# Performance work log

Measured on AMD Instinct MI355X. Metric: run time of the kernel, lower is better.

Reference implementation:

```python
import jax, jax.numpy as jnp
import numpy as np

B, IN, OUT, D = 8192, 1024, 1024, 8


def setup_inputs() -> dict:
    key = jax.random.key(0)
    k1, k2, k3, k4 = jax.random.split(key, 4)
    # kaiming-uniform-ish init for weights, uniform for biases (values don't affect correctness)
    bound = 1.0 / np.sqrt(IN)
    return {
        "input": jax.random.normal(k1, (B, IN), dtype=jnp.float32),
        "w": jax.random.uniform(k2, (B, D), dtype=jnp.float32),
        "weights": jax.random.uniform(k3, (D, OUT, IN), dtype=jnp.float32, minval=-bound, maxval=bound),
        "biases": jax.random.uniform(k4, (D, OUT), dtype=jnp.float32, minval=-bound, maxval=bound),
    }


def reference(input, w, weights, biases):
    # Original math: weight[b] = sum_d w[b,d] * weights[d]  (shape [out,in])
    #                out[b]    = input[b] @ weight[b].T + sum_d w[b,d]*biases[d]
    # Restructured as one big GEMM + cheap dsize reduction:
    # tmp[b,d,o] = sum_i input[b,i] * weights[d,o,i]   (GEMM: [B,in] x [in, d*out])
    tmp = jnp.einsum('bi,doi->bdo', input, weights)
    out = jnp.einsum('bdo,bd->bo', tmp, w) + w @ biases
    return out
```

## Files before the change

kernel.cpp:

```cpp
#include <hip/hip_runtime.h>
#include <stdint.h>

typedef unsigned short u16;
typedef float v4f __attribute__((ext_vector_type(4)));
typedef short v8s __attribute__((ext_vector_type(8)));

#define B_   8192
#define IN_  1024
#define OUT_ 1024
#define D_   8

#define BM 128
#define BN 128
#define BK 64
#define KROW (D_ * IN_)

__device__ __forceinline__ u16 f2bf(float f) {
  uint32_t u = __float_as_uint(f);
  u += 0x7fffu + ((u >> 16) & 1u);
  return (u16)(u >> 16);
}

__global__ __launch_bounds__(256) void prep_fused(
    const float* __restrict__ input, const float* __restrict__ w,
    const float* __restrict__ weights,
    u16* __restrict__ aS, u16* __restrict__ wtBf) {
  const int bid = blockIdx.x;
  const int tid = threadIdx.x;
  if (bid < 8192) {
    const int b  = bid;
    const int i4 = tid;
    float4 v = ((const float4*)(input + (size_t)b * IN_))[i4];
    const float* wr_ = w + (size_t)b * D_;
    ushort4* dst = (ushort4*)aS + (size_t)b * (KROW / 4);
#pragma unroll
    for (int d = 0; d < D_; ++d) {
      const float s = wr_[d];
      ushort4 o;
      o.x = f2bf(s * v.x); o.y = f2bf(s * v.y);
      o.z = f2bf(s * v.z); o.w = f2bf(s * v.w);
      dst[d * (IN_ / 4) + i4] = o;
    }
  } else {
    int idx = (bid - 8192) * 256 + tid;
    float4 v = ((const float4*)weights)[idx];
    ushort4 o;
    o.x = f2bf(v.x); o.y = f2bf(v.y); o.z = f2bf(v.z); o.w = f2bf(v.w);
    ((ushort4*)wtBf)[idx] = o;
  }
}

__device__ __forceinline__ void gload_lds16(const u16* g, u16* l) {
  typedef __attribute__((address_space(1))) void gvoid;
  typedef __attribute__((address_space(3))) void lvoid;
  __builtin_amdgcn_global_load_lds((gvoid*)g, (lvoid*)l, 16, 0, 0);
}

__global__ __launch_bounds__(256) void gemm_main(
    const u16* __restrict__ A,
    const u16* __restrict__ Wt,
    const float* __restrict__ w,
    const float* __restrict__ biases,
    float* __restrict__ out) {
  __shared__ __align__(16) u16 As[BM * BK];
  __shared__ __align__(16) u16 Bs[BN * BK];

  const int id   = blockIdx.x;
  const int xcd  = id & 7;
  const int slot = id >> 3;
  const int by   = xcd + ((slot & 7) << 3);
  const int bx   = slot >> 3;

  const int tid  = threadIdx.x;
  const int wid  = tid >> 6;
  const int lane = tid & 63;
  const int wr   = wid >> 1, wc = wid & 1;
  const int quad = lane >> 4, l16 = lane & 15;
  const int m0   = by * BM;
  const int n0   = bx * BN;

  const int swz  = (lane & 7) ^ ((lane >> 3) & 7);
  const int rowS = wid * 32 + (lane >> 3);
  const u16* aBase[4];
  const u16* bBase[4];
  u16* lA[4];
  u16* lB[4];
#pragma unroll
  for (int j = 0; j < 4; ++j) {
    const int row = rowS + j * 8;
    aBase[j] = A  + (size_t)(m0 + row) * KROW + swz * 8;
    bBase[j] = Wt + (size_t)(n0 + row) * IN_  + swz * 8;
    const int c = wid * 256 + j * 64 + lane;
    lA[j] = As + c * 8;
    lB[j] = Bs + c * 8;
  }

  const int aRow = wr * 64 + l16;
  const int bRow = wc * 64 + l16;
  const int e    = l16 & 7;
  int aC[2], bC[2];
#pragma unroll
  for (int h = 0; h < 2; ++h) {
    aC[h] = ((quad + 4 * h) ^ e) * 8;
    bC[h] = aC[h];
  }

  const v4f vzero = {0.f, 0.f, 0.f, 0.f};
  v4f acc[4][4];
#pragma unroll
  for (int mt = 0; mt < 4; ++mt)
#pragma unroll
    for (int nt = 0; nt < 4; ++nt) acc[mt][nt] = vzero;

  for (int dd = 0; dd < D_; ++dd) {
    const size_t aOffG = (size_t)dd * IN_;
    const size_t bOffG = (size_t)dd * OUT_ * IN_;
    for (int it = 0; it < IN_ / BK; ++it) {
      const int i0 = it * BK;
#pragma unroll
      for (int j = 0; j < 4; ++j) gload_lds16(aBase[j] + aOffG + i0, lA[j]);
#pragma unroll
      for (int j = 0; j < 4; ++j) gload_lds16(bBase[j] + bOffG + i0, lB[j]);
      __builtin_amdgcn_s_waitcnt(0);
      __syncthreads();

#pragma unroll
      for (int h = 0; h < 2; ++h) {
        v8s af[4], bf[4];
#pragma unroll
        for (int mt = 0; mt < 4; ++mt)
          af[mt] = *(const v8s*)(As + (aRow + mt * 16) * BK + aC[h]);
#pragma unroll
        for (int nt = 0; nt < 4; ++nt)
          bf[nt] = *(const v8s*)(Bs + (bRow + nt * 16) * BK + bC[h]);
#pragma unroll
        for (int mt = 0; mt < 4; ++mt)
#pragma unroll
          for (int nt = 0; nt < 4; ++nt)
            acc[mt][nt] = __builtin_amdgcn_mfma_f32_16x16x32_bf16(
                af[mt], bf[nt], acc[mt][nt], 0, 0, 0);
      }
      __syncthreads();
    }
  }

  float bcol[4][8];
#pragma unroll
  for (int nt = 0; nt < 4; ++nt) {
    const int col = n0 + wc * 64 + nt * 16 + l16;
#pragma unroll
    for (int dd = 0; dd < 8; ++dd) bcol[nt][dd] = biases[dd * OUT_ + col];
  }
#pragma unroll
  for (int mt = 0; mt < 4; ++mt) {
#pragma unroll
    for (int r = 0; r < 4; ++r) {
      const int grow = m0 + wr * 64 + mt * 16 + quad * 4 + r;
      const v4f* wp = (const v4f*)(w + (size_t)grow * D_);
      const v4f wa = wp[0], wb = wp[1];
#pragma unroll
      for (int nt = 0; nt < 4; ++nt) {
        const int col = n0 + wc * 64 + nt * 16 + l16;
        const float bias = wa[0] * bcol[nt][0] + wa[1] * bcol[nt][1] +
                           wa[2] * bcol[nt][2] + wa[3] * bcol[nt][3] +
                           wb[0] * bcol[nt][4] + wb[1] * bcol[nt][5] +
                           wb[2] * bcol[nt][6] + wb[3] * bcol[nt][7];
        out[(size_t)grow * OUT_ + col] = acc[mt][nt][r] + bias;
      }
    }
  }
}

#define FBK 32
__global__ __launch_bounds__(256) void convert_both(
    const float* __restrict__ input, const float* __restrict__ weights,
    u16* __restrict__ inBf, u16* __restrict__ wtBf) {
  int i4 = blockIdx.x * blockDim.x + threadIdx.x;
  const int n4 = (B_ * IN_) / 4;
  const float* src;
  u16* dst;
  int idx;
  if (i4 < n4) { src = input;   dst = inBf; idx = i4; }
  else         { src = weights; dst = wtBf; idx = i4 - n4; }
  float4 v = ((const float4*)src)[idx];
  ushort4 o;
  o.x = f2bf(v.x); o.y = f2bf(v.y); o.z = f2bf(v.z); o.w = f2bf(v.w);
  ((ushort4*)dst)[idx] = o;
}

__global__ __launch_bounds__(256) void gemm_fallback(
    const u16* __restrict__ A, const u16* __restrict__ Wt,
    const float* __restrict__ w, const float* __restrict__ biases,
    float* __restrict__ out) {
  __shared__ __align__(16) u16 As[BM * FBK];
  __shared__ __align__(16) u16 Bs[BN * FBK];
  const int tid  = threadIdx.x;
  const int wid  = tid >> 6;
  const int lane = tid & 63;
  const int wr   = wid >> 1, wc = wid & 1;
  const int quad = lane >> 4, l16 = lane & 15;
  const int m0   = blockIdx.y * BM;
  const int n0   = blockIdx.x * BN;
  const int c0  = wid * 128 + lane;
  const int c1  = c0 + 64;
  const int rA0 = c0 >> 2, cA0 = (c0 & 3) << 3;
  const int rA1 = c1 >> 2, cA1 = (c1 & 3) << 3;
  const u16* aP0 = A + (size_t)(m0 + rA0) * IN_ + cA0;
  const u16* aP1 = A + (size_t)(m0 + rA1) * IN_ + cA1;
  const u16* bB0 = Wt + (size_t)(n0 + rA0) * IN_ + cA0;
  const u16* bB1 = Wt + (size_t)(n0 + rA1) * IN_ + cA1;
  u16* lA0 = As + c0 * 8;
  u16* lA1 = As + c1 * 8;
  u16* lB0 = Bs + c0 * 8;
  u16* lB1 = Bs + c1 * 8;
  const int aOff = (wr * 64 + l16) * FBK + quad * 8;
  const int bOff = (wc * 64 + l16) * FBK + quad * 8;
  const v4f vzero = {0.f, 0.f, 0.f, 0.f};
  v4f fin[4][4];
#pragma unroll
  for (int mt = 0; mt < 4; ++mt)
#pragma unroll
    for (int nt = 0; nt < 4; ++nt) fin[mt][nt] = vzero;
  for (int d = 0; d < D_; ++d) {
    const u16* bP0 = bB0 + (size_t)d * OUT_ * IN_;
    const u16* bP1 = bB1 + (size_t)d * OUT_ * IN_;
    v4f acc[4][4];
#pragma unroll
    for (int mt = 0; mt < 4; ++mt)
#pragma unroll
      for (int nt = 0; nt < 4; ++nt) acc[mt][nt] = vzero;
    for (int it = 0; it < 32; ++it) {
      const int i0 = it * FBK;
      gload_lds16(aP0 + i0, lA0);
      gload_lds16(aP1 + i0, lA1);
      gload_lds16(bP0 + i0, lB0);
      gload_lds16(bP1 + i0, lB1);
      __builtin_amdgcn_s_waitcnt(0);
      __syncthreads();
      v8s af[4], bf[4];
#pragma unroll
      for (int mt = 0; mt < 4; ++mt)
        af[mt] = *(const v8s*)(As + aOff + mt * 16 * FBK);
#pragma unroll
      for (int nt = 0; nt < 4; ++nt)
        bf[nt] = *(const v8s*)(Bs + bOff + nt * 16 * FBK);
#pragma unroll
      for (int mt = 0; mt < 4; ++mt)
#pragma unroll
        for (int nt = 0; nt < 4; ++nt)
          acc[mt][nt] = __builtin_amdgcn_mfma_f32_16x16x32_bf16(
              af[mt], bf[nt], acc[mt][nt], 0, 0, 0);
      __syncthreads();
    }
#pragma unroll
    for (int mt = 0; mt < 4; ++mt) {
      const int rowb = m0 + wr * 64 + mt * 16 + quad * 4;
#pragma unroll
      for (int r = 0; r < 4; ++r) {
        const float ws_ = w[(size_t)(rowb + r) * D_ + d];
#pragma unroll
        for (int nt = 0; nt < 4; ++nt) fin[mt][nt][r] += ws_ * acc[mt][nt][r];
      }
    }
  }
  float bcol[4][8];
#pragma unroll
  for (int nt = 0; nt < 4; ++nt) {
    const int col = n0 + wc * 64 + nt * 16 + l16;
#pragma unroll
    for (int dd = 0; dd < 8; ++dd) bcol[nt][dd] = biases[dd * OUT_ + col];
  }
#pragma unroll
  for (int mt = 0; mt < 4; ++mt) {
#pragma unroll
    for (int r = 0; r < 4; ++r) {
      const int grow = m0 + wr * 64 + mt * 16 + quad * 4 + r;
      const v4f* wp = (const v4f*)(w + (size_t)grow * D_);
      const v4f wa = wp[0], wb = wp[1];
#pragma unroll
      for (int nt = 0; nt < 4; ++nt) {
        const int col = n0 + wc * 64 + nt * 16 + l16;
        const float bias = wa[0] * bcol[nt][0] + wa[1] * bcol[nt][1] +
                           wa[2] * bcol[nt][2] + wa[3] * bcol[nt][3] +
                           wb[0] * bcol[nt][4] + wb[1] * bcol[nt][5] +
                           wb[2] * bcol[nt][6] + wb[3] * bcol[nt][7];
        out[(size_t)grow * OUT_ + col] = fin[mt][nt][r] + bias;
      }
    }
  }
}

extern "C" void kernel_launch(void* const* d_in, const int* in_sizes, int n_in,
                              void* d_out, int out_size, void* d_ws, size_t ws_size,
                              hipStream_t stream) {
  const float* input   = (const float*)d_in[0];
  const float* w       = (const float*)d_in[1];
  const float* weights = (const float*)d_in[2];
  const float* biases  = (const float*)d_in[3];
  float* out = (float*)d_out;

  const size_t aS_bytes = (size_t)B_ * KROW * 2;
  const size_t wt_bytes = (size_t)D_ * OUT_ * IN_ * 2;

  if (ws_size >= aS_bytes + wt_bytes) {
    u16* aS   = (u16*)d_ws;
    u16* wtBf = (u16*)((char*)d_ws + aS_bytes);
    prep_fused<<<dim3(16384), 256, 0, stream>>>(input, w, weights, aS, wtBf);
    gemm_main<<<dim3(512), 256, 0, stream>>>(aS, wtBf, w, biases, out);
  } else {
    u16* inBf = (u16*)d_ws;
    u16* wtBf = inBf + (size_t)B_ * IN_;
    const int totalF4 = (B_ * IN_ + D_ * OUT_ * IN_) / 4;
    convert_both<<<dim3(totalF4 / 256), 256, 0, stream>>>(input, weights, inBf, wtBf);
    gemm_fallback<<<dim3(OUT_ / BN, B_ / BM), 256, 0, stream>>>(inBf, wtBf, w, biases, out);
  }
}
```

Before: 250.3 us.

## Replace w-scaled expanded A with per-d GEMM and fp32 w-weighted accumulation

Stops materialising the w-scaled input copy [B, D*IN] in bf16 and instead converts the input once to [B, IN]. The main kernel runs a per-d GEMM into a temporary accumulator and folds it into the final result scaled by w[b,d] in fp32. This cuts prep-kernel writes and the A-operand footprint eightfold, so the A tile is reused across all d from cache. It costs an extra accumulator register set and epilogue FMAs per d, and removes the workspace-size fallback path.

```diff
diff --git a/kernel.cpp b/kernel.cpp
--- a/kernel.cpp
+++ b/kernel.cpp
@@ -13,7 +13,6 @@
 #define BM 128
 #define BN 128
 #define BK 64
-#define KROW (D_ * IN_)
 
 __device__ __forceinline__ u16 f2bf(float f) {
   uint32_t u = __float_as_uint(f);
@@ -21,33 +20,20 @@
   return (u16)(u >> 16);
 }
 
-__global__ __launch_bounds__(256) void prep_fused(
-    const float* __restrict__ input, const float* __restrict__ w,
-    const float* __restrict__ weights,
-    u16* __restrict__ aS, u16* __restrict__ wtBf) {
-  const int bid = blockIdx.x;
-  const int tid = threadIdx.x;
-  if (bid < 8192) {
-    const int b  = bid;
-    const int i4 = tid;
-    float4 v = ((const float4*)(input + (size_t)b * IN_))[i4];
-    const float* wr_ = w + (size_t)b * D_;
-    ushort4* dst = (ushort4*)aS + (size_t)b * (KROW / 4);
-#pragma unroll
-    for (int d = 0; d < D_; ++d) {
-      const float s = wr_[d];
-      ushort4 o;
-      o.x = f2bf(s * v.x); o.y = f2bf(s * v.y);
-      o.z = f2bf(s * v.z); o.w = f2bf(s * v.w);
-      dst[d * (IN_ / 4) + i4] = o;
-    }
-  } else {
-    int idx = (bid - 8192) * 256 + tid;
-    float4 v = ((const float4*)weights)[idx];
-    ushort4 o;
-    o.x = f2bf(v.x); o.y = f2bf(v.y); o.z = f2bf(v.z); o.w = f2bf(v.w);
-    ((ushort4*)wtBf)[idx] = o;
-  }
+__global__ __launch_bounds__(256) void convert_both(
+    const float* __restrict__ input, const float* __restrict__ weights,
+    u16* __restrict__ inBf, u16* __restrict__ wtBf) {
+  int i4 = blockIdx.x * blockDim.x + threadIdx.x;
+  const int n4 = (B_ * IN_) / 4;
+  const float* src;
+  u16* dst;
+  int idx;
+  if (i4 < n4) { src = input;   dst = inBf; idx = i4; }
+  else         { src = weights; dst = wtBf; idx = i4 - n4; }
+  float4 v = ((const float4*)src)[idx];
+  ushort4 o;
+  o.x = f2bf(v.x); o.y = f2bf(v.y); o.z = f2bf(v.z); o.w = f2bf(v.w);
+  ((ushort4*)dst)[idx] = o;
 }
 
 __device__ __forceinline__ void gload_lds16(const u16* g, u16* l) {
@@ -56,7 +42,7 @@
   __builtin_amdgcn_global_load_lds((gvoid*)g, (lvoid*)l, 16, 0, 0);
 }
 
-__global__ __launch_bounds__(256) void gemm_main(
+__global__ __launch_bounds__(256) void gemm_perd(
     const u16* __restrict__ A,
     const u16* __restrict__ Wt,
     const float* __restrict__ w,
@@ -88,8 +74,8 @@
 #pragma unroll
   for (int j = 0; j < 4; ++j) {
     const int row = rowS + j * 8;
-    aBase[j] = A  + (size_t)(m0 + row) * KROW + swz * 8;
-    bBase[j] = Wt + (size_t)(n0 + row) * IN_  + swz * 8;
+    aBase[j] = A  + (size_t)(m0 + row) * IN_ + swz * 8;
+    bBase[j] = Wt + (size_t)(n0 + row) * IN_ + swz * 8;
     const int c = wid * 256 + j * 64 + lane;
     lA[j] = As + c * 8;
     lB[j] = Bs + c * 8;
@@ -106,19 +92,24 @@
   }
 
   const v4f vzero = {0.f, 0.f, 0.f, 0.f};
-  v4f acc[4][4];
+  v4f fin[4][4];
 #pragma unroll
   for (int mt = 0; mt < 4; ++mt)
 #pragma unroll
-    for (int nt = 0; nt < 4; ++nt) acc[mt][nt] = vzero;
+    for (int nt = 0; nt < 4; ++nt) fin[mt][nt] = vzero;
 
   for (int dd = 0; dd < D_; ++dd) {
-    const size_t aOffG = (size_t)dd * IN_;
     const size_t bOffG = (size_t)dd * OUT_ * IN_;
+    v4f acc[4][4];
+#pragma unroll
+    for (int mt = 0; mt < 4; ++mt)
+#pragma unroll
+      for (int nt = 0; nt < 4; ++nt) acc[mt][nt] = vzero;
+
     for (int it = 0; it < IN_ / BK; ++it) {
       const int i0 = it * BK;
 #pragma unroll
-      for (int j = 0; j < 4; ++j) gload_lds16(aBase[j] + aOffG + i0, lA[j]);
+      for (int j = 0; j < 4; ++j) gload_lds16(aBase[j] + i0, lA[j]);
 #pragma unroll
       for (int j = 0; j < 4; ++j) gload_lds16(bBase[j] + bOffG + i0, lB[j]);
       __builtin_amdgcn_s_waitcnt(0);
@@ -142,127 +133,19 @@
       }
       __syncthreads();
     }
-  }
 
-  float bcol[4][8];
-#pragma unroll
-  for (int nt = 0; nt < 4; ++nt) {
-    const int col = n0 + wc * 64 + nt * 16 + l16;
-#pragma unroll
-    for (int dd = 0; dd < 8; ++dd) bcol[nt][dd] = biases[dd * OUT_ + col];
-  }
-#pragma unroll
-  for (int mt = 0; mt < 4; ++mt) {
-#pragma unroll
-    for (int r = 0; r < 4; ++r) {
-      const int grow = m0 + wr * 64 + mt * 16 + quad * 4 + r;
-      const v4f* wp = (const v4f*)(w + (size_t)grow * D_);
-      const v4f wa = wp[0], wb = wp[1];
-#pragma unroll
-      for (int nt = 0; nt < 4; ++nt) {
-        const int col = n0 + wc * 64 + nt * 16 + l16;
-        const float bias = wa[0] * bcol[nt][0] + wa[1] * bcol[nt][1] +
-                           wa[2] * bcol[nt][2] + wa[3] * bcol[nt][3] +
-                           wb[0] * bcol[nt][4] + wb[1] * bcol[nt][5] +
-                           wb[2] * bcol[nt][6] + wb[3] * bcol[nt][7];
-        out[(size_t)grow * OUT_ + col] = acc[mt][nt][r] + bias;
-      }
-    }
-  }
-}
-
-#define FBK 32
-__global__ __launch_bounds__(256) void convert_both(
-    const float* __restrict__ input, const float* __restrict__ weights,
-    u16* __restrict__ inBf, u16* __restrict__ wtBf) {
-  int i4 = blockIdx.x * blockDim.x + threadIdx.x;
-  const int n4 = (B_ * IN_) / 4;
-  const float* src;
-  u16* dst;
-  int idx;
-  if (i4 < n4) { src = input;   dst = inBf; idx = i4; }
-  else         { src = weights; dst = wtBf; idx = i4 - n4; }
-  float4 v = ((const float4*)src)[idx];
-  ushort4 o;
-  o.x = f2bf(v.x); o.y = f2bf(v.y); o.z = f2bf(v.z); o.w = f2bf(v.w);
-  ((ushort4*)dst)[idx] = o;
-}
-
-__global__ __launch_bounds__(256) void gemm_fallback(
-    const u16* __restrict__ A, const u16* __restrict__ Wt,
-    const float* __restrict__ w, const float* __restrict__ biases,
-    float* __restrict__ out) {
-  __shared__ __align__(16) u16 As[BM * FBK];
-  __shared__ __align__(16) u16 Bs[BN * FBK];
-  const int tid  = threadIdx.x;
-  const int wid  = tid >> 6;
-  const int lane = tid & 63;
-  const int wr   = wid >> 1, wc = wid & 1;
-  const int quad = lane >> 4, l16 = lane & 15;
-  const int m0   = blockIdx.y * BM;
-  const int n0   = blockIdx.x * BN;
-  const int c0  = wid * 128 + lane;
-  const int c1  = c0 + 64;
-  const int rA0 = c0 >> 2, cA0 = (c0 & 3) << 3;
-  const int rA1 = c1 >> 2, cA1 = (c1 & 3) << 3;
-  const u16* aP0 = A + (size_t)(m0 + rA0) * IN_ + cA0;
-  const u16* aP1 = A + (size_t)(m0 + rA1) * IN_ + cA1;
-  const u16* bB0 = Wt + (size_t)(n0 + rA0) * IN_ + cA0;
-  const u16* bB1 = Wt + (size_t)(n0 + rA1) * IN_ + cA1;
-  u16* lA0 = As + c0 * 8;
-  u16* lA1 = As + c1 * 8;
-  u16* lB0 = Bs + c0 * 8;
-  u16* lB1 = Bs + c1 * 8;
-  const int aOff = (wr * 64 + l16) * FBK + quad * 8;
-  const int bOff = (wc * 64 + l16) * FBK + quad * 8;
-  const v4f vzero = {0.f, 0.f, 0.f, 0.f};
-  v4f fin[4][4];
-#pragma unroll
-  for (int mt = 0; mt < 4; ++mt)
-#pragma unroll
-    for (int nt = 0; nt < 4; ++nt) fin[mt][nt] = vzero;
-  for (int d = 0; d < D_; ++d) {
-    const u16* bP0 = bB0 + (size_t)d * OUT_ * IN_;
-    const u16* bP1 = bB1 + (size_t)d * OUT_ * IN_;
-    v4f acc[4][4];
-#pragma unroll
-    for (int mt = 0; mt < 4; ++mt)
-#pragma unroll
-      for (int nt = 0; nt < 4; ++nt) acc[mt][nt] = vzero;
-    for (int it = 0; it < 32; ++it) {
-      const int i0 = it * FBK;
-      gload_lds16(aP0 + i0, lA0);
-      gload_lds16(aP1 + i0, lA1);
-      gload_lds16(bP0 + i0, lB0);
-      gload_lds16(bP1 + i0, lB1);
-      __builtin_amdgcn_s_waitcnt(0);
-      __syncthreads();
-      v8s af[4], bf[4];
-#pragma unroll
-      for (int mt = 0; mt < 4; ++mt)
-        af[mt] = *(const v8s*)(As + aOff + mt * 16 * FBK);
-#pragma unroll
-      for (int nt = 0; nt < 4; ++nt)
-        bf[nt] = *(const v8s*)(Bs + bOff + nt * 16 * FBK);
-#pragma unroll
-      for (int mt = 0; mt < 4; ++mt)
-#pragma unroll
-        for (int nt = 0; nt < 4; ++nt)
-          acc[mt][nt] = __builtin_amdgcn_mfma_f32_16x16x32_bf16(
-              af[mt], bf[nt], acc[mt][nt], 0, 0, 0);
-      __syncthreads();
-    }
 #pragma unroll
     for (int mt = 0; mt < 4; ++mt) {
       const int rowb = m0 + wr * 64 + mt * 16 + quad * 4;
 #pragma unroll
       for (int r = 0; r < 4; ++r) {
-        const float ws_ = w[(size_t)(rowb + r) * D_ + d];
+        const float ws_ = w[(size_t)(rowb + r) * D_ + dd];
 #pragma unroll
         for (int nt = 0; nt < 4; ++nt) fin[mt][nt][r] += ws_ * acc[mt][nt][r];
       }
     }
   }
+
   float bcol[4][8];
 #pragma unroll
   for (int nt = 0; nt < 4; ++nt) {
@@ -299,19 +182,10 @@
   const float* biases  = (const float*)d_in[3];
   float* out = (float*)d_out;
 
-  const size_t aS_bytes = (size_t)B_ * KROW * 2;
-  const size_t wt_bytes = (size_t)D_ * OUT_ * IN_ * 2;
+  u16* inBf = (u16*)d_ws;
+  u16* wtBf = inBf + (size_t)B_ * IN_;
 
-  if (ws_size >= aS_bytes + wt_bytes) {
-    u16* aS   = (u16*)d_ws;
-    u16* wtBf = (u16*)((char*)d_ws + aS_bytes);
-    prep_fused<<<dim3(16384), 256, 0, stream>>>(input, w, weights, aS, wtBf);
-    gemm_main<<<dim3(512), 256, 0, stream>>>(aS, wtBf, w, biases, out);
-  } else {
-    u16* inBf = (u16*)d_ws;
-    u16* wtBf = inBf + (size_t)B_ * IN_;
-    const int totalF4 = (B_ * IN_ + D_ * OUT_ * IN_) / 4;
-    convert_both<<<dim3(totalF4 / 256), 256, 0, stream>>>(input, weights, inBf, wtBf);
-    gemm_fallback<<<dim3(OUT_ / BN, B_ / BM), 256, 0, stream>>>(inBf, wtBf, w, biases, out);
-  }
+  const int totalF4 = (B_ * IN_ + D_ * OUT_ * IN_) / 4;
+  convert_both<<<dim3(totalF4 / 256), 256, 0, stream>>>(input, weights, inBf, wtBf);
+  gemm_perd<<<dim3(512), 256, 0, stream>>>(inBf, wtBf, w, biases, out);
 }
```

New measurement: 362.2 us. +44.7%, slower.
